# Kernel optimization log

Hardware: AMD Instinct MI355X
Metric: run time of the kernel (lower is better)

The kernel has to match this reference:

```python
import jax, jax.numpy as jnp
import numpy as np
import math

D_MODEL = 1024
N_HEADS = 16
Q_PROJ = D_MODEL // 4
KV_PROJ = D_MODEL // 4
DH = D_MODEL // N_HEADS
LN_EPS = 1e-5


def _layernorm(x, gamma, beta):
    mu = jnp.mean(x, axis=-1, keepdims=True)
    var = jnp.mean(jnp.square(x - mu), axis=-1, keepdims=True)
    return (x - mu) * jax.lax.rsqrt(var + LN_EPS) * gamma + beta


def setup_inputs() -> dict:
    key = jax.random.key(0)
    ks = jax.random.split(key, 7)
    B, S = 2, 2048
    x = jax.random.normal(ks[0], (B, S, D_MODEL), dtype=jnp.float32)
    W_dq = 0.01 * jax.random.normal(ks[1], (D_MODEL, Q_PROJ), dtype=jnp.float32)
    W_uq = 0.01 * jax.random.normal(ks[2], (Q_PROJ, D_MODEL), dtype=jnp.float32)
    W_dkv = 0.01 * jax.random.normal(ks[3], (D_MODEL, KV_PROJ), dtype=jnp.float32)
    W_ukv = 0.01 * jax.random.normal(ks[4], (KV_PROJ, 2 * D_MODEL), dtype=jnp.float32)
    W_o = 0.01 * jax.random.normal(ks[5], (D_MODEL, D_MODEL), dtype=jnp.float32)
    return {
        "x": x,
        "W_dq": W_dq, "W_uq": W_uq,
        "q_ln_g": jnp.ones((Q_PROJ,), jnp.float32), "q_ln_b": jnp.zeros((Q_PROJ,), jnp.float32),
        "W_dkv": W_dkv, "W_ukv": W_ukv,
        "kv_ln_g": jnp.ones((KV_PROJ,), jnp.float32), "kv_ln_b": jnp.zeros((KV_PROJ,), jnp.float32),
        "W_o": W_o,
    }


def reference(x, W_dq, W_uq, q_ln_g, q_ln_b, W_dkv, W_ukv, kv_ln_g, kv_ln_b, W_o):
    B, S, D = x.shape
    # low-rank Q path
    cq = _layernorm(x @ W_dq, q_ln_g, q_ln_b)          # [B,S,q_proj]
    Q = cq @ W_uq                                       # [B,S,D]
    # low-rank KV path
    ckv = _layernorm(x @ W_dkv, kv_ln_g, kv_ln_b)       # [B,S,kv_proj]
    KV = ckv @ W_ukv                                    # [B,S,2D]
    K, V = KV[..., :D], KV[..., D:]
    q = Q.reshape(B, S, N_HEADS, DH)
    k = K.reshape(B, S, N_HEADS, DH)
    v = V.reshape(B, S, N_HEADS, DH)
    scores = jnp.einsum("bqhd,bkhd->bhqk", q, k) / math.sqrt(float(DH))
    # faithful to original: multiply by tril mask, then set exact zeros to -inf
    mask = jnp.tril(jnp.ones((S, S), dtype=scores.dtype))
    scores = scores * mask
    scores = jnp.where(scores == 0, -jnp.inf, scores)
    attn = jax.nn.softmax(scores, axis=-1)
    out = jnp.einsum("bhqk,bkhd->bqhd", attn, v).reshape(B, S, D)
    return out @ W_o.T
```

## Files before the change

### kernel.cpp

```cpp
#include <hip/hip_runtime.h>

typedef __bf16 bf16;
typedef __bf16 bf16x4 __attribute__((ext_vector_type(4)));
typedef __bf16 bf16x8 __attribute__((ext_vector_type(8)));
typedef float f32x4 __attribute__((ext_vector_type(4)));

#define D_MODEL 1024
#define PROJ    256
#define SEQ     2048
#define BATCH   2
#define TOK     4096
#define NH      16
#define DH      64
#define NEG_BIG (-1e30f)
#define QSCALE  0.18033688011112042f

#if __has_builtin(__builtin_amdgcn_exp2f)
#define EXP2(x) __builtin_amdgcn_exp2f(x)
#else
#define EXP2(x) exp2f(x)
#endif

typedef __attribute__((address_space(3))) unsigned int  lds_u32;
typedef __attribute__((address_space(1))) unsigned int  glb_u32;

__device__ __forceinline__ void gl2lds16(const void* gsrc, void* ldst) {
    __builtin_amdgcn_global_load_lds((const glb_u32*)gsrc, (lds_u32*)ldst, 16, 0, 0);
}

#define VM_WAIT(N) asm volatile("s_waitcnt vmcnt(" #N ")" ::: "memory")
#define LGKM0      asm volatile("s_waitcnt lgkmcnt(0)" ::: "memory")
#define SCHEDB()   __builtin_amdgcn_sched_barrier(0)
#define SBAR()     __builtin_amdgcn_s_barrier()

template <int CTRL>
__device__ __forceinline__ float dppmov(float x) {
    int i = __builtin_bit_cast(int, x);
    i = __builtin_amdgcn_update_dpp(i, i, CTRL, 0xf, 0xf, false);
    return __builtin_bit_cast(float, i);
}
__device__ __forceinline__ float rowsum16(float v) {
    v += dppmov<0xB1>(v);
    v += dppmov<0x4E>(v);
    v += dppmov<0x141>(v);
    v += dppmov<0x140>(v);
    return v;
}

__global__ __launch_bounds__(256) void prep_kernel(
    const float* __restrict__ W_o, const float* __restrict__ x,
    const float* __restrict__ W_dq, const float* __restrict__ W_dkv,
    const float* __restrict__ W_uq, const float* __restrict__ W_ukv,
    bf16* __restrict__ Wo16, bf16* __restrict__ x16,
    bf16* __restrict__ Wt_dq, bf16* __restrict__ Wt_dkv,
    bf16* __restrict__ Wt_uq, bf16* __restrict__ Wt_ukv) {
    if (blockIdx.x < 320) {
        __shared__ float tile[64][65];
        int t = blockIdx.x;
        const float* src; bf16* dst; int R, C;
        if (t < 64)       { src = W_dq;  dst = Wt_dq;  R = 1024; C = 256; }
        else if (t < 128) { src = W_dkv; dst = Wt_dkv; R = 1024; C = 256;  t -= 64; }
        else if (t < 192) { src = W_uq;  dst = Wt_uq;  R = 256;  C = 1024; t -= 128; }
        else              { src = W_ukv; dst = Wt_ukv; R = 256;  C = 2048; t -= 192; }
        const int tilesC = C >> 6;
        const int r0 = (t / tilesC) << 6;
        const int c0 = (t % tilesC) << 6;
        const int tr = threadIdx.x >> 6;
        const int tc = threadIdx.x & 63;
#pragma unroll
        for (int i = 0; i < 16; ++i)
            tile[tr * 16 + i][tc] = src[(size_t)(r0 + tr * 16 + i) * C + c0 + tc];
        __syncthreads();
#pragma unroll
        for (int i = 0; i < 16; ++i)
            dst[(size_t)(c0 + tr * 16 + i) * R + r0 + tc] =
                (bf16)tile[tc][tr * 16 + i];
    } else {
        const int NW = 262144;
        const int NX = 1048576;
        for (int i = (blockIdx.x - 320) * 256 + threadIdx.x; i < NW + NX;
             i += 1024 * 256) {
            if (i < NW) {
                float4 v = ((const float4*)W_o)[i];
                bf16x4 p;
                p[0] = (bf16)v.x; p[1] = (bf16)v.y;
                p[2] = (bf16)v.z; p[3] = (bf16)v.w;
                ((bf16x4*)Wo16)[i] = p;
            } else {
                int j = i - NW;
                float4 v = ((const float4*)x)[j];
                bf16x4 p;
                p[0] = (bf16)v.x; p[1] = (bf16)v.y;
                p[2] = (bf16)v.z; p[3] = (bf16)v.w;
                ((bf16x4*)x16)[j] = p;
            }
        }
    }
}

__global__ __launch_bounds__(512) void gemm_ln_kernel(
    const bf16* __restrict__ x16,
    const bf16* __restrict__ Wt_q, const bf16* __restrict__ Wt_kv,
    const float* __restrict__ q_g, const float* __restrict__ q_b,
    const float* __restrict__ kv_g, const float* __restrict__ kv_b,
    bf16* __restrict__ cq, bf16* __restrict__ ckv) {
    __shared__ alignas(16) bf16 xA[3][32 * 32];
    __shared__ alignas(16) bf16 wB[3][256 * 32];
    __shared__ float red1[8][16];
    __shared__ float red2[8][16];

    const int K = 1024;
    const bf16* Wt = blockIdx.y ? Wt_kv : Wt_q;
    const float* gamma = blockIdx.y ? kv_g : q_g;
    const float* beta  = blockIdx.y ? kv_b : q_b;
    bf16* out = blockIdx.y ? ckv : cq;

    const int m0 = blockIdx.x * 32;
    const int wv = threadIdx.x >> 6;
    const int lane = threadIdx.x & 63;
    const int g = lane >> 4;
    const int ln16 = lane & 15;
    const int wr = wv >> 2;
    const int wc = wv & 3;

    const int crow = lane >> 2;
    const int ckc = lane & 3;
    const bf16* gx0 = x16 + (size_t)(m0 + crow) * K + ckc * 8;
    const bf16* gx1 = x16 + (size_t)(m0 + 16 + crow) * K + ckc * 8;
    const bf16* gw0 = Wt + (size_t)(32 * wv + crow) * K + ckc * 8;
    const bf16* gw1 = Wt + (size_t)(32 * wv + 16 + crow) * K + ckc * 8;

    f32x4 acc[4] = {};
    const int nst = K >> 5;

#pragma unroll
    for (int s = 0; s < 2; ++s) {
        gl2lds16(gx0 + s * 32, (char*)xA + s * 2048);
        gl2lds16(gx1 + s * 32, (char*)xA + s * 2048 + 1024);
        gl2lds16(gw0 + s * 32, (char*)wB + s * 16384 + wv * 2048);
        gl2lds16(gw1 + s * 32, (char*)wB + s * 16384 + wv * 2048 + 1024);
    }
    VM_WAIT(0); SCHEDB(); SBAR();

    for (int s = 0; s < nst; ++s) {
        if (s > 0) {
            if (s + 1 < nst) { VM_WAIT(4); } else { VM_WAIT(0); }
            SCHEDB(); SBAR();
        }
        if (s + 2 < nst) {
            const int b3 = (s + 2) % 3;
            const int k2 = (s + 2) * 32;
            gl2lds16(gx0 + k2, (char*)xA + b3 * 2048);
            gl2lds16(gx1 + k2, (char*)xA + b3 * 2048 + 1024);
            gl2lds16(gw0 + k2, (char*)wB + b3 * 16384 + wv * 2048);
            gl2lds16(gw1 + k2, (char*)wB + b3 * 16384 + wv * 2048 + 1024);
        }
        const bf16* cx = &xA[s % 3][0];
        const bf16* cw = &wB[s % 3][0];
        bf16x8 a = *(const bf16x8*)(cx + (wr * 16 + ln16) * 32 + g * 8);
        bf16x8 bb[4];
#pragma unroll
        for (int t = 0; t < 4; ++t)
            bb[t] = *(const bf16x8*)(cw + (wc * 64 + 16 * t + ln16) * 32 + g * 8);
        __builtin_amdgcn_s_setprio(1);
#pragma unroll
        for (int t = 0; t < 4; ++t)
            acc[t] = __builtin_amdgcn_mfma_f32_16x16x32_bf16(a, bb[t], acc[t], 0, 0, 0);
        __builtin_amdgcn_s_setprio(0);
    }

    float s1[4], s2[4];
#pragma unroll
    for (int r = 0; r < 4; ++r) {
        float a = 0.f, b = 0.f;
#pragma unroll
        for (int t = 0; t < 4; ++t) { float v = acc[t][r]; a += v; b += v * v; }
        s1[r] = rowsum16(a); s2[r] = rowsum16(b);
    }
    if (ln16 == 0) {
#pragma unroll
        for (int r = 0; r < 4; ++r) {
            red1[wv][g * 4 + r] = s1[r];
            red2[wv][g * 4 + r] = s2[r];
        }
    }
    __syncthreads();
#pragma unroll
    for (int r = 0; r < 4; ++r) {
        int rl = g * 4 + r;
        float t1 = red1[wr * 4 + 0][rl] + red1[wr * 4 + 1][rl] +
                   red1[wr * 4 + 2][rl] + red1[wr * 4 + 3][rl];
        float t2 = red2[wr * 4 + 0][rl] + red2[wr * 4 + 1][rl] +
                   red2[wr * 4 + 2][rl] + red2[wr * 4 + 3][rl];
        float mu = t1 * (1.0f / 256.0f);
        float var = t2 * (1.0f / 256.0f) - mu * mu;
        float rs = rsqrtf(var + 1e-5f);
        int row = m0 + wr * 16 + rl;
#pragma unroll
        for (int t = 0; t < 4; ++t) {
            int col = wc * 64 + 16 * t + ln16;
            float v = (acc[t][r] - mu) * rs * gamma[col] + beta[col];
            out[(size_t)row * PROJ + col] = (bf16)v;
        }
    }
}

__device__ __forceinline__ void gemm_body128(
    const bf16* __restrict__ A, const bf16* __restrict__ Bt,
    bf16* __restrict__ C, bf16* __restrict__ C2, int K,
    int bx, int by, int mode, bf16* tA, bf16* tB) {
    const int w = threadIdx.x >> 6;
    const int lane = threadIdx.x & 63;
    const int g = lane >> 4;
    const int ln16 = lane & 15;
    const int wr = w >> 1;
    const int wc = w & 1;

    const int m0 = bx * 128;
    const int n0 = by * 128;

    const int crow = lane >> 2;
    const int ckc = lane & 3;
    const bf16* gA0 = A  + (size_t)(m0 + 32 * w + crow) * K + ckc * 8;
    const bf16* gA1 = gA0 + (size_t)16 * K;
    const bf16* gB0 = Bt + (size_t)(n0 + 32 * w + crow) * K + ckc * 8;
    const bf16* gB1 = gB0 + (size_t)16 * K;

    f32x4 acc[4][4] = {};
    const int nst = K >> 5;

#pragma unroll
    for (int s = 0; s < 2; ++s) {
        gl2lds16(gA0 + s * 32, (char*)tA + s * 8192 + w * 2048);
        gl2lds16(gA1 + s * 32, (char*)tA + s * 8192 + w * 2048 + 1024);
        gl2lds16(gB0 + s * 32, (char*)tB + s * 8192 + w * 2048);
        gl2lds16(gB1 + s * 32, (char*)tB + s * 8192 + w * 2048 + 1024);
    }
    VM_WAIT(0); SCHEDB(); SBAR();

    for (int s = 0; s < nst; ++s) {
        if (s > 0) {
            if (s + 1 < nst) { VM_WAIT(4); } else { VM_WAIT(0); }
            SCHEDB(); SBAR();
        }
        if (s + 2 < nst) {
            const int b3 = (s + 2) % 3;
            const int k2 = (s + 2) * 32;
            gl2lds16(gA0 + k2, (char*)tA + b3 * 8192 + w * 2048);
            gl2lds16(gA1 + k2, (char*)tA + b3 * 8192 + w * 2048 + 1024);
            gl2lds16(gB0 + k2, (char*)tB + b3 * 8192 + w * 2048);
            gl2lds16(gB1 + k2, (char*)tB + b3 * 8192 + w * 2048 + 1024);
        }
        const bf16* cA = tA + (s % 3) * 4096;
        const bf16* cB = tB + (s % 3) * 4096;

        bf16x8 af[4], bfr[4];
#pragma unroll
        for (int q = 0; q < 4; ++q)
            af[q] = *(const bf16x8*)(cA + (wr * 64 + q * 16 + ln16) * 32 + g * 8);
#pragma unroll
        for (int t = 0; t < 4; ++t)
            bfr[t] = *(const bf16x8*)(cB + (wc * 64 + t * 16 + ln16) * 32 + g * 8);
        __builtin_amdgcn_s_setprio(1);
#pragma unroll
        for (int q = 0; q < 4; ++q)
#pragma unroll
            for (int t = 0; t < 4; ++t)
                acc[q][t] = __builtin_amdgcn_mfma_f32_16x16x32_bf16(
                    af[q], bfr[t], acc[q][t], 0, 0, 0);
        __builtin_amdgcn_s_setprio(0);
    }

#pragma unroll
    for (int q = 0; q < 4; ++q)
#pragma unroll
        for (int t = 0; t < 4; ++t) {
            const int col = n0 + wc * 64 + t * 16 + ln16;
            const int tok0 = m0 + wr * 64 + q * 16 + g * 4;
            if (mode == 2 && col >= 1024) {
                int cc = col - 1024;
                int h = cc >> 6, d = cc & 63;
                int b = tok0 >> 11, sq = tok0 & 2047;
                bf16x4 pk;
#pragma unroll
                for (int r = 0; r < 4; ++r) pk[r] = (bf16)acc[q][t][r];
                *(bf16x4*)(C2 + ((size_t)((b * 16 + h) * 64 + d) * SEQ + sq)) = pk;
            } else {
#pragma unroll
                for (int r = 0; r < 4; ++r) {
                    int row = tok0 + r;
                    float v = acc[q][t][r];
                    if (mode == 1) v *= QSCALE;
                    int h = col >> 6, d = col & 63;
                    int b = row >> 11, sq = row & 2047;
                    C[((size_t)((b * 16 + h) * 2048 + sq)) * 64 + d] = (bf16)v;
                }
            }
        }
}

__global__ __launch_bounds__(256) void gemm_qkv_kernel(
    const bf16* __restrict__ cq, const bf16* __restrict__ Wt_uq,
    const bf16* __restrict__ ckv, const bf16* __restrict__ Wt_ukv,
    bf16* __restrict__ Qh, bf16* __restrict__ Kh, bf16* __restrict__ Vt) {
    __shared__ alignas(16) bf16 tA[3][128 * 32];
    __shared__ alignas(16) bf16 tB[3][128 * 32];
    const int i = blockIdx.x;
    if (i < 256) {
        gemm_body128(cq, Wt_uq, Qh, nullptr, PROJ,
                     i >> 3, i & 7, 1, &tA[0][0], &tB[0][0]);
    } else {
        const int j = i - 256;
        gemm_body128(ckv, Wt_ukv, Kh, Vt, PROJ,
                     j >> 4, j & 15, 2, &tA[0][0], &tB[0][0]);
    }
}

__device__ __forceinline__ void gemm_body(
    const bf16* __restrict__ A, const bf16* __restrict__ Bt,
    float* __restrict__ C, int N, int K,
    int bx, int by, bf16* tA, bf16* tB) {
    const int w = threadIdx.x >> 6;
    const int lane = threadIdx.x & 63;
    const int g = lane >> 4;
    const int ln16 = lane & 15;
    const int wr = w >> 1;
    const int wc = w & 1;

    const int m0 = bx * 64;
    const int n0 = by * 128;

    const int crow = lane >> 2;
    const int ckc = lane & 3;
    const bf16* gA  = A  + (size_t)(m0 + w * 16 + crow) * K + ckc * 8;
    const bf16* gB0 = Bt + (size_t)(n0 + w * 16 + crow) * K + ckc * 8;
    const bf16* gB1 = Bt + (size_t)(n0 + 64 + w * 16 + crow) * K + ckc * 8;

    f32x4 acc[2][4] = {};
    const int nst = K >> 5;

#pragma unroll
    for (int s = 0; s < 2; ++s) {
        gl2lds16(gA + s * 32, (char*)tA + s * 4096 + w * 1024);
        gl2lds16(gB0 + s * 32, (char*)tB + s * 8192 + w * 1024);
        gl2lds16(gB1 + s * 32, (char*)tB + s * 8192 + 4096 + w * 1024);
    }
    VM_WAIT(0); SCHEDB(); SBAR();

    for (int s = 0; s < nst; ++s) {
        if (s > 0) {
            if (s + 1 < nst) { VM_WAIT(3); } else { VM_WAIT(0); }
            SCHEDB(); SBAR();
        }
        if (s + 2 < nst) {
            const int b3 = (s + 2) % 3;
            const int k2 = (s + 2) * 32;
            gl2lds16(gA + k2, (char*)tA + b3 * 4096 + w * 1024);
            gl2lds16(gB0 + k2, (char*)tB + b3 * 8192 + w * 1024);
            gl2lds16(gB1 + k2, (char*)tB + b3 * 8192 + 4096 + w * 1024);
        }
        const bf16* cA = tA + (s % 3) * 2048;
        const bf16* cB = tB + (s % 3) * 4096;

        bf16x8 af[2], bfr[4];
#pragma unroll
        for (int q = 0; q < 2; ++q)
            af[q] = *(const bf16x8*)(cA + (wr * 32 + q * 16 + ln16) * 32 + g * 8);
#pragma unroll
        for (int t = 0; t < 4; ++t)
            bfr[t] = *(const bf16x8*)(cB + (wc * 64 + t * 16 + ln16) * 32 + g * 8);
        __builtin_amdgcn_s_setprio(1);
#pragma unroll
        for (int q = 0; q < 2; ++q)
#pragma unroll
            for (int t = 0; t < 4; ++t)
                acc[q][t] = __builtin_amdgcn_mfma_f32_16x16x32_bf16(
                    af[q], bfr[t], acc[q][t], 0, 0, 0);
        __builtin_amdgcn_s_setprio(0);
    }

#pragma unroll
    for (int q = 0; q < 2; ++q)
#pragma unroll
        for (int t = 0; t < 4; ++t) {
            const int col = n0 + wc * 64 + t * 16 + ln16;
            const int tok0 = m0 + wr * 32 + q * 16 + g * 4;
#pragma unroll
            for (int r = 0; r < 4; ++r)
                C[(size_t)(tok0 + r) * N + col] = acc[q][t][r];
        }
}

__global__ __launch_bounds__(256) void gemm_o_kernel(
    const bf16* __restrict__ A, const bf16* __restrict__ Bt,
    float* __restrict__ C, int M, int N, int K) {
    __shared__ alignas(16) bf16 tA[3][64 * 32];
    __shared__ alignas(16) bf16 tB[3][128 * 32];
    gemm_body(A, Bt, C, N, K, blockIdx.x, blockIdx.y, &tA[0][0], &tB[0][0]);
}

__device__ __forceinline__ void qk_exp_pack(
    int k0, int q, bool masked, int g, int ln16,
    bf16x8 aq0, bf16x8 aq1, const bf16x8* Kf,
    bf16x8& P1, bf16x8& P2) {
    f32x4 sc[4];
    __builtin_amdgcn_s_setprio(1);
#pragma unroll
    for (int c = 0; c < 4; ++c) {
        f32x4 z = {};
        z = __builtin_amdgcn_mfma_f32_16x16x32_bf16(Kf[2 * c], aq0, z, 0, 0, 0);
        z = __builtin_amdgcn_mfma_f32_16x16x32_bf16(Kf[2 * c + 1], aq1, z, 0, 0, 0);
        sc[c] = z;
    }
    __builtin_amdgcn_s_setprio(0);
    if (masked) {
        const int kb = k0 + 8 * g;
#pragma unroll
        for (int c = 0; c < 4; ++c)
#pragma unroll
            for (int r = 0; r < 4; ++r) {
                int kcol = kb + (c & 1) * 4 + r + ((c >> 1) << 5);
                if (kcol > q) sc[c][r] = NEG_BIG;
            }
    }
#pragma unroll
    for (int c = 0; c < 4; ++c)
#pragma unroll
        for (int r = 0; r < 4; ++r) sc[c][r] = EXP2(sc[c][r]);
#pragma unroll
    for (int r = 0; r < 4; ++r) {
        P1[r] = (bf16)sc[0][r]; P1[4 + r] = (bf16)sc[1][r];
        P2[r] = (bf16)sc[2][r]; P2[4 + r] = (bf16)sc[3][r];
    }
}

__device__ __forceinline__ void pv_accum(
    bf16x8 P1, bf16x8 P2, const bf16x8* Vf, bf16x8 vones,
    f32x4* o, f32x4& oli) {
    __builtin_amdgcn_s_setprio(1);
#pragma unroll
    for (int t = 0; t < 4; ++t) {
        o[t] = __builtin_amdgcn_mfma_f32_16x16x32_bf16(Vf[2 * t], P1, o[t], 0, 0, 0);
        o[t] = __builtin_amdgcn_mfma_f32_16x16x32_bf16(Vf[2 * t + 1], P2, o[t], 0, 0, 0);
    }
    oli = __builtin_amdgcn_mfma_f32_16x16x32_bf16(vones, P1, oli, 0, 0, 0);
    oli = __builtin_amdgcn_mfma_f32_16x16x32_bf16(vones, P2, oli, 0, 0, 0);
    __builtin_amdgcn_s_setprio(0);
}

__global__ __launch_bounds__(256) void attn_kernel(
    const bf16* __restrict__ Qh, const bf16* __restrict__ Kh,
    const bf16* __restrict__ Vt, bf16* __restrict__ AT) {
    __shared__ alignas(128) bf16 kbuf[2][64 * 64];
    __shared__ alignas(128) bf16 vbuf[2][64 * 64];

    const int lane = threadIdx.x & 63;
    const int g = lane >> 4;
    const int ln16 = lane & 15;
    const int wv = threadIdx.x >> 6;

    const int bh = blockIdx.x & 31;
    const int qsuper = 31 - (blockIdx.x >> 5);
    const int nt = qsuper + 1;
    const int qb = qsuper * 64 + wv * 16;
    const int q = qb + ln16;

    const bf16* Kbh = Kh + (size_t)bh * SEQ * DH;
    const bf16* Vbh = Vt + (size_t)bh * DH * SEQ;

    const int rho = lane >> 3;
    const int sl  = lane & 7;
    int kofs[2];
    size_t vofs[2];
#pragma unroll
    for (int i = 0; i < 2; ++i) {
        const int row = 16 * wv + 8 * i + rho;
        const int c = sl ^ ((rho & 3) | ((i & 1) << 2));
        kofs[i] = row * 64 + c * 8;
        vofs[i] = (size_t)row * SEQ + c * 8;
    }

    const int row_base = ((ln16 & 12) << 1) + (ln16 & 3);
    int kro[4], vro[4];
#pragma unroll
    for (int c = 0; c < 4; ++c) {
        const int row = row_base + (c & 1) * 4 + ((c >> 1) << 5);
        const int fr = (row & 3) | (((row >> 3) & 1) << 2);
        kro[c] = row * 128 + (g ^ fr) * 16;
    }
#pragma unroll
    for (int t = 0; t < 4; ++t) {
        const int d = 16 * t + ln16;
        const int fd = (d & 3) | (((d >> 3) & 1) << 2);
        vro[t] = d * 128 + (g ^ fd) * 16;
    }

    const bf16* qp = Qh + ((size_t)bh * SEQ + q) * DH + g * 8;
    bf16x8 aq0 = *(const bf16x8*)qp, aq1 = *(const bf16x8*)(qp + 32);

    bf16x8 vones;
#pragma unroll
    for (int i = 0; i < 8; ++i) vones[i] = (bf16)1.0f;

    f32x4 o[4] = {};
    f32x4 oli = {};

    {
        const int t1 = (nt > 1) ? 1 : 0;
#pragma unroll
        for (int i = 0; i < 2; ++i) {
            gl2lds16(Kbh + kofs[i], (char*)kbuf + wv * 2048 + i * 1024);
            gl2lds16(Vbh + vofs[i], (char*)vbuf + wv * 2048 + i * 1024);
        }
#pragma unroll
        for (int i = 0; i < 2; ++i) {
            gl2lds16(Kbh + (size_t)t1 * 64 * 64 + kofs[i],
                     (char*)kbuf + 8192 + wv * 2048 + i * 1024);
            gl2lds16(Vbh + vofs[i] + (size_t)t1 * 64,
                     (char*)vbuf + 8192 + wv * 2048 + i * 1024);
        }
    }
    VM_WAIT(0); SCHEDB(); SBAR();

    for (int kt = 0; kt < nt; ++kt) {
        if (kt > 0) {
            if (kt + 1 < nt) { VM_WAIT(4); } else { VM_WAIT(0); }
            SCHEDB(); SBAR();
        }
        const char* kb = (const char*)kbuf + (kt & 1) * 8192;
        const char* vb = (const char*)vbuf + (kt & 1) * 8192;
        bf16x8 Kf[8], Vf[8];
#pragma unroll
        for (int c = 0; c < 4; ++c) {
            Kf[2 * c]     = *(const bf16x8*)(kb + kro[c]);
            Kf[2 * c + 1] = *(const bf16x8*)(kb + (kro[c] ^ 64));
        }
#pragma unroll
        for (int t = 0; t < 4; ++t) {
            Vf[2 * t]     = *(const bf16x8*)(vb + vro[t]);
            Vf[2 * t + 1] = *(const bf16x8*)(vb + (vro[t] ^ 64));
        }
        LGKM0; SCHEDB(); SBAR();
        if (kt + 2 < nt) {
            const size_t k0n = (size_t)(kt + 2) * 64;
            char* kd = (char*)kbuf + (kt & 1) * 8192 + wv * 2048;
            char* vd = (char*)vbuf + (kt & 1) * 8192 + wv * 2048;
#pragma unroll
            for (int i = 0; i < 2; ++i) {
                gl2lds16(Kbh + k0n * 64 + kofs[i], kd + i * 1024);
                gl2lds16(Vbh + vofs[i] + k0n, vd + i * 1024);
            }
        }

        bf16x8 P1, P2;
        qk_exp_pack(kt * 64, q, kt == qsuper, g, ln16, aq0, aq1, Kf, P1, P2);
        pv_accum(P1, P2, Vf, vones, o, oli);
    }

    const float inv = 1.0f / oli[0];
    const int b = bh >> 4, h = bh & 15;
    const size_t tok = (size_t)(b * SEQ + q) * D_MODEL + h * DH;
#pragma unroll
    for (int t = 0; t < 4; ++t) {
        bf16x4 pk;
#pragma unroll
        for (int r = 0; r < 4; ++r) pk[r] = (bf16)(o[t][r] * inv);
        *(bf16x4*)(AT + tok + 16 * t + 4 * g) = pk;
    }
}

extern "C" void kernel_launch(void* const* d_in, const int* in_sizes, int n_in,
                              void* d_out, int out_size, void* d_ws, size_t ws_size,
                              hipStream_t stream) {
    const float* x     = (const float*)d_in[0];
    const float* W_dq  = (const float*)d_in[1];
    const float* W_uq  = (const float*)d_in[2];
    const float* q_g   = (const float*)d_in[3];
    const float* q_b   = (const float*)d_in[4];
    const float* W_dkv = (const float*)d_in[5];
    const float* W_ukv = (const float*)d_in[6];
    const float* kv_g  = (const float*)d_in[7];
    const float* kv_b  = (const float*)d_in[8];
    const float* W_o   = (const float*)d_in[9];

    char* ws = (char*)d_ws;
    size_t off = 0;
    bf16* Wo16   = (bf16*)(ws + off); off += (size_t)D_MODEL * D_MODEL * 2;
    bf16* Wt_dq  = (bf16*)(ws + off); off += (size_t)PROJ * D_MODEL * 2;
    bf16* Wt_dkv = (bf16*)(ws + off); off += (size_t)PROJ * D_MODEL * 2;
    bf16* Wt_uq  = (bf16*)(ws + off); off += (size_t)D_MODEL * PROJ * 2;
    bf16* Wt_ukv = (bf16*)(ws + off); off += (size_t)(2 * D_MODEL) * PROJ * 2;
    bf16* x16    = (bf16*)(ws + off); off += (size_t)TOK * D_MODEL * 2;
    bf16* cq     = (bf16*)(ws + off); off += (size_t)TOK * PROJ * 2;
    bf16* ckv    = (bf16*)(ws + off); off += (size_t)TOK * PROJ * 2;
    bf16* Qh     = (bf16*)(ws + off); off += (size_t)TOK * D_MODEL * 2;
    bf16* Kh     = (bf16*)(ws + off); off += (size_t)TOK * D_MODEL * 2;
    bf16* Vt     = (bf16*)(ws + off); off += (size_t)TOK * D_MODEL * 2;
    bf16* AT     = (bf16*)(ws + off); off += (size_t)TOK * D_MODEL * 2;

    prep_kernel<<<1344, 256, 0, stream>>>(
        W_o, x, W_dq, W_dkv, W_uq, W_ukv,
        Wo16, x16, Wt_dq, Wt_dkv, Wt_uq, Wt_ukv);

    gemm_ln_kernel<<<dim3(TOK / 32, 2), 512, 0, stream>>>(
        x16, Wt_dq, Wt_dkv, q_g, q_b, kv_g, kv_b, cq, ckv);

    gemm_qkv_kernel<<<768, 256, 0, stream>>>(cq, Wt_uq, ckv, Wt_ukv, Qh, Kh, Vt);

    attn_kernel<<<1024, 256, 0, stream>>>(Qh, Kh, Vt, AT);

    gemm_o_kernel<<<dim3(TOK / 64, D_MODEL / 128), 256, 0, stream>>>(
        AT, Wo16, (float*)d_out, TOK, D_MODEL, D_MODEL);
}
```

Baseline: 174.1 us.

## Widen attention blocks to 128 queries with eight waves sharing K/V tiles

Each attention block now covers 128 query rows with 8 waves instead of 64 rows with 4 waves. The K/V tile load per stage is split across twice as many waves, so each wave issues one copy per buffer instead of two. Waves whose rows lie entirely before a key tile skip compute, and the diagonal mask is chosen per wave. This halves the number of blocks and K/V tile reloads, which cuts global and LDS traffic. The cost is fewer blocks, coarser causal load balancing, and idle waves on the diagonal tiles.

```diff
diff --git a/kernel.cpp b/kernel.cpp
--- a/kernel.cpp
+++ b/kernel.cpp
@@ -448,7 +448,7 @@
     __builtin_amdgcn_s_setprio(0);
 }
 
-__global__ __launch_bounds__(256) void attn_kernel(
+__global__ __launch_bounds__(512) void attn_kernel(
     const bf16* __restrict__ Qh, const bf16* __restrict__ Kh,
     const bf16* __restrict__ Vt, bf16* __restrict__ AT) {
     __shared__ alignas(128) bf16 kbuf[2][64 * 64];
@@ -460,9 +460,10 @@
     const int wv = threadIdx.x >> 6;
 
     const int bh = blockIdx.x & 31;
-    const int qsuper = 31 - (blockIdx.x >> 5);
-    const int nt = qsuper + 1;
-    const int qb = qsuper * 64 + wv * 16;
+    const int j = blockIdx.x >> 5;
+    const int super = (j < 8) ? 15 - j : j - 8;
+    const int nt = 2 * super + 2;
+    const int qb = super * 128 + wv * 16;
     const int q = qb + ln16;
 
     const bf16* Kbh = Kh + (size_t)bh * SEQ * DH;
@@ -470,15 +471,10 @@
 
     const int rho = lane >> 3;
     const int sl  = lane & 7;
-    int kofs[2];
-    size_t vofs[2];
-#pragma unroll
-    for (int i = 0; i < 2; ++i) {
-        const int row = 16 * wv + 8 * i + rho;
-        const int c = sl ^ ((rho & 3) | ((i & 1) << 2));
-        kofs[i] = row * 64 + c * 8;
-        vofs[i] = (size_t)row * SEQ + c * 8;
-    }
+    const int srow = 8 * wv + rho;
+    const int sc8 = sl ^ ((rho & 3) | ((wv & 1) << 2));
+    const int kofs = srow * 64 + sc8 * 8;
+    const size_t vofs = (size_t)srow * SEQ + sc8 * 8;
 
     const int row_base = ((ln16 & 12) << 1) + (ln16 & 3);
     int kro[4], vro[4];
@@ -505,26 +501,15 @@
     f32x4 o[4] = {};
     f32x4 oli = {};
 
-    {
-        const int t1 = (nt > 1) ? 1 : 0;
-#pragma unroll
-        for (int i = 0; i < 2; ++i) {
-            gl2lds16(Kbh + kofs[i], (char*)kbuf + wv * 2048 + i * 1024);
-            gl2lds16(Vbh + vofs[i], (char*)vbuf + wv * 2048 + i * 1024);
-        }
-#pragma unroll
-        for (int i = 0; i < 2; ++i) {
-            gl2lds16(Kbh + (size_t)t1 * 64 * 64 + kofs[i],
-                     (char*)kbuf + 8192 + wv * 2048 + i * 1024);
-            gl2lds16(Vbh + vofs[i] + (size_t)t1 * 64,
-                     (char*)vbuf + 8192 + wv * 2048 + i * 1024);
-        }
-    }
+    gl2lds16(Kbh + kofs, (char*)kbuf + wv * 1024);
+    gl2lds16(Vbh + vofs, (char*)vbuf + wv * 1024);
+    gl2lds16(Kbh + (size_t)64 * 64 + kofs, (char*)kbuf + 8192 + wv * 1024);
+    gl2lds16(Vbh + vofs + 64, (char*)vbuf + 8192 + wv * 1024);
     VM_WAIT(0); SCHEDB(); SBAR();
 
     for (int kt = 0; kt < nt; ++kt) {
         if (kt > 0) {
-            if (kt + 1 < nt) { VM_WAIT(4); } else { VM_WAIT(0); }
+            if (kt + 1 < nt) { VM_WAIT(2); } else { VM_WAIT(0); }
             SCHEDB(); SBAR();
         }
         const char* kb = (const char*)kbuf + (kt & 1) * 8192;
@@ -543,18 +528,18 @@
         LGKM0; SCHEDB(); SBAR();
         if (kt + 2 < nt) {
             const size_t k0n = (size_t)(kt + 2) * 64;
-            char* kd = (char*)kbuf + (kt & 1) * 8192 + wv * 2048;
-            char* vd = (char*)vbuf + (kt & 1) * 8192 + wv * 2048;
-#pragma unroll
-            for (int i = 0; i < 2; ++i) {
-                gl2lds16(Kbh + k0n * 64 + kofs[i], kd + i * 1024);
-                gl2lds16(Vbh + vofs[i] + k0n, vd + i * 1024);
-            }
-        }
-
-        bf16x8 P1, P2;
-        qk_exp_pack(kt * 64, q, kt == qsuper, g, ln16, aq0, aq1, Kf, P1, P2);
-        pv_accum(P1, P2, Vf, vones, o, oli);
+            gl2lds16(Kbh + k0n * 64 + kofs,
+                     (char*)kbuf + (kt & 1) * 8192 + wv * 1024);
+            gl2lds16(Vbh + vofs + k0n,
+                     (char*)vbuf + (kt & 1) * 8192 + wv * 1024);
+        }
+
+        if (64 * kt <= qb + 15) {
+            const bool msk = (64 * (kt + 1) > qb);
+            bf16x8 P1, P2;
+            qk_exp_pack(kt * 64, q, msk, g, ln16, aq0, aq1, Kf, P1, P2);
+            pv_accum(P1, P2, Vf, vones, o, oli);
+        }
     }
 
     const float inv = 1.0f / oli[0];
@@ -607,7 +592,7 @@
 
     gemm_qkv_kernel<<<768, 256, 0, stream>>>(cq, Wt_uq, ckv, Wt_ukv, Qh, Kh, Vt);
 
-    attn_kernel<<<1024, 256, 0, stream>>>(Qh, Kh, Vt, AT);
+    attn_kernel<<<512, 512, 0, stream>>>(Qh, Kh, Vt, AT);
 
     gemm_o_kernel<<<dim3(TOK / 64, D_MODEL / 128), 256, 0, stream>>>(
         AT, Wo16, (float*)d_out, TOK, D_MODEL, D_MODEL);
```

After: 186.6 us. 7.2% more time.
